# Optimization experiments

Hardware: AMD Instinct MI355X
Metric: run time of the kernel (lower is better)

Reference implementation:

```python
import jax, jax.numpy as jnp
import numpy as np

EPS = 1e-5
P = 2  # polynomial kernel degree


def setup_inputs() -> dict:
    key = jax.random.key(0)
    k1, k2, k3 = jax.random.split(key, 3)
    b, t, h, d = 2, 2048, 8, 64
    Q = jax.random.normal(k1, (b, t, h, d), jnp.float32)
    K = jax.random.normal(k2, (b, t, h, d), jnp.float32)
    V = jax.random.normal(k3, (b, t, h, d), jnp.float32)
    return {"Q": Q, "K": K, "V": V, "chunk_count": 16}


def reference(Q, K, V, chunk_count):
    b, t, h, d = Q.shape
    dv = V.shape[-1]
    c = chunk_count
    n = t // c  # tokens per chunk

    def to_chunked(X):
        # [b, t, h, d] -> [c, b, h, n, d]
        return X.reshape(b, c, n, h, X.shape[-1]).transpose(1, 0, 3, 2, 4)

    Qc, Kc, Vc = to_chunked(Q), to_chunked(K), to_chunked(V)

    # ---- per-chunk states: s = K^T K, S = sum_n (K_n outer K_n) outer V_n ----
    s_loc = jnp.einsum('cbhni,cbhnj->cbhij', Kc, Kc)                 # [c,b,h,d,d]
    S_loc = jnp.einsum('cbhni,cbhnj,cbhnv->cbhijv', Kc, Kc, Vc)      # [c,b,h,d,d,dv]
    # inclusive cumulative merge over chunks
    S = jnp.cumsum(S_loc, axis=0)
    s = jnp.cumsum(s_loc, axis=0)

    # ---- local within-chunk masked quadratic attention ----
    D = jnp.einsum('cbhqi,cbhki->cbhqk', Qc, Kc)                     # [c,b,h,n,n]
    C = D ** P
    mask = jnp.tril(jnp.ones((n, n), dtype=bool))
    B = jnp.where(mask, C, 0.0)
    Y = jnp.einsum('cbhqk,cbhkv->cbhqv', B, Vc)                      # [c,b,h,n,dv]
    Z = B.sum(-1) + EPS                                              # [c,b,h,n]

    # ---- cross-chunk contribution: chunk i>0 attends to state of chunks <i ----
    Qp = Qc[1:]
    Sp, sp = S[:-1], s[:-1]
    num = jnp.einsum('cbhni,cbhnj,cbhijv->cbhnv', Qp, Qp, Sp)
    den = jnp.einsum('cbhni,cbhnj,cbhij->cbhn', Qp, Qp, sp)
    Y = Y.at[1:].add(num)
    Z = Z.at[1:].add(den)

    out = (Y / Z[..., None]).transpose(1, 0, 3, 2, 4).reshape(b, t, h, dv)
    return out
```

## Files before the change

### kernel.cpp

```cpp
#include <hip/hip_runtime.h>
#include <hip/hip_fp16.h>

typedef __attribute__((ext_vector_type(8))) _Float16 f16x8;
typedef __attribute__((ext_vector_type(4))) _Float16 f16x4;
typedef __attribute__((ext_vector_type(8))) unsigned short u16x8;
typedef __attribute__((ext_vector_type(4))) float f32x4;

constexpr int NT = 256;
constexpr int TILE_SHORTS = 4096;

__device__ __forceinline__ int swzoff(int row, int c) {
    return row * 64 + ((c ^ (row & 7)) << 3);
}
__device__ __forceinline__ unsigned short f2h_u(float x) {
    return __half_as_ushort(__float2half(x));
}

__global__ __launch_bounds__(256, 4) void prepass(
    const float* __restrict__ Kg, const float* __restrict__ Vg,
    unsigned short* __restrict__ Kw, unsigned short* __restrict__ Vw)
{
    __shared__ __align__(16) float Vl[64 * 68];
    const int tile = blockIdx.x;
    const int bh   = blockIdx.y;
    const int b = bh >> 3, h = bh & 7;
    const int tid = threadIdx.x;
    const size_t gbase = (((size_t)b * 2048 + tile * 64) * 8 + h) * 64;

    #pragma unroll
    for (int j = 0; j < 4; ++j) {
        int id = j * 256 + tid, row = id >> 4, c4 = id & 15;
        *(float4*)&Vl[row * 68 + c4 * 4] =
            *(const float4*)&Vg[gbase + (size_t)row * 512 + c4 * 4];
    }

    unsigned short* Ko = Kw + (size_t)(bh * 32 + tile) * TILE_SHORTS;
    #pragma unroll
    for (int j = 0; j < 2; ++j) {
        int id = j * 256 + tid, row = id >> 3, c = id & 7;
        const float* src = &Kg[gbase + (size_t)row * 512 + c * 8];
        float4 x = *(const float4*)src, y = *(const float4*)(src + 4);
        u16x8 o;
        o[0] = f2h_u(x.x); o[1] = f2h_u(x.y); o[2] = f2h_u(x.z); o[3] = f2h_u(x.w);
        o[4] = f2h_u(y.x); o[5] = f2h_u(y.y); o[6] = f2h_u(y.z); o[7] = f2h_u(y.w);
        *(u16x8*)&Ko[swzoff(row, c)] = o;
    }
    __syncthreads();

    unsigned short* Vo = Vw + (size_t)(bh * 32 + tile) * TILE_SHORTS;
    #pragma unroll
    for (int j = 0; j < 2; ++j) {
        int id = j * 256 + tid, vrow = id >> 3, g = id & 7;
        u16x8 o;
        #pragma unroll
        for (int jj = 0; jj < 8; ++jj) {
            int kk = ((g & 1) * 2 + (jj >> 2)) * 16 + (g >> 1) * 4 + (jj & 3);
            o[jj] = f2h_u(Vl[kk * 68 + vrow]);
        }
        *(u16x8*)&Vo[swzoff(vrow, g)] = o;
    }
}

__global__ __launch_bounds__(NT, 3) void attn_pow2_f16(
    const float* __restrict__ Qg,
    const unsigned short* __restrict__ Kw, const unsigned short* __restrict__ Vw,
    float* __restrict__ Og)
{
    __shared__ __align__(16) unsigned short lds[4 * TILE_SHORTS];
    unsigned short* const Kb = lds;
    unsigned short* const Vb = lds + 2 * TILE_SHORTS;
    const int tid  = threadIdx.x;
    const int lane = tid & 63;
    const int wave = tid >> 6;
    const int a    = lane & 15;
    const int quad = lane >> 4;
    const int m0   = wave * 16;

    int r0 = (int)blockIdx.x;
    int wr = (r0 < 256) ? r0 : (767 - r0);
    const int qt = 31 - (wr >> 4);
    const int bh = wr & 15;
    const int b = bh >> 3, h = bh & 7;
    const int q0 = qt * 64;

    f16x8 bQ[2];
    {
        const size_t qrowbase = (((size_t)b * 2048 + q0 + m0 + a) * 8 + h) * 64;
        #pragma unroll
        for (int ks = 0; ks < 2; ++ks) {
            const float* src = &Qg[qrowbase + ks * 32 + quad * 8];
            float4 x = *(const float4*)src, y = *(const float4*)(src + 4);
            u16x8 o;
            o[0] = f2h_u(x.x); o[1] = f2h_u(x.y); o[2] = f2h_u(x.z); o[3] = f2h_u(x.w);
            o[4] = f2h_u(y.x); o[5] = f2h_u(y.y); o[6] = f2h_u(y.z); o[7] = f2h_u(y.w);
            bQ[ks] = __builtin_bit_cast(f16x8, o);
        }
    }

    const unsigned short* Ktiles = Kw + (size_t)bh * 32 * TILE_SHORTS;
    const unsigned short* Vtiles = Vw + (size_t)bh * 32 * TILE_SHORTS;

    u16x8 rK[2], rV[2];
    auto gload = [&](int kt) {
        const u16x8* kg = (const u16x8*)(Ktiles + (size_t)kt * TILE_SHORTS);
        const u16x8* vg = (const u16x8*)(Vtiles + (size_t)kt * TILE_SHORTS);
        rK[0] = kg[tid * 2]; rK[1] = kg[tid * 2 + 1];
        rV[0] = vg[tid * 2]; rV[1] = vg[tid * 2 + 1];
    };
    gload(0);

    f32x4 oacc[4];
    #pragma unroll
    for (int n = 0; n < 4; ++n) oacc[n] = (f32x4){0.f, 0.f, 0.f, 0.f};
    float den_l = 0.f;

    union U8 { u16x8 u; f16x4 q[2]; };

    for (int kt = 0; kt <= qt; ++kt) {
        const int buf = kt & 1;
        u16x8* kd = (u16x8*)(Kb + buf * TILE_SHORTS);
        u16x8* vd = (u16x8*)(Vb + buf * TILE_SHORTS);
        kd[tid * 2] = rK[0]; kd[tid * 2 + 1] = rK[1];
        vd[tid * 2] = rV[0]; vd[tid * 2 + 1] = rV[1];
        __syncthreads();
        if (kt < qt) gload(kt + 1);

        const unsigned short* Kc = Kb + buf * TILE_SHORTS;
        const unsigned short* Vc = Vb + buf * TILE_SHORTS;

        f32x4 sacc[4];
        #pragma unroll
        for (int s = 0; s < 4; ++s) sacc[s] = (f32x4){0.f, 0.f, 0.f, 0.f};
        #pragma unroll
        for (int s = 0; s < 4; ++s) {
            #pragma unroll
            for (int ks = 0; ks < 2; ++ks) {
                f16x8 aK = *(const f16x8*)&Kc[swzoff(s * 16 + a, ks * 4 + quad)];
                sacc[s] = __builtin_amdgcn_mfma_f32_16x16x32_f16(aK, bQ[ks], sacc[s], 0, 0, 0);
            }
        }

        const bool diag = (kt == qt);
        f16x4 aS[4];
        #pragma unroll
        for (int s = 0; s < 4; ++s) {
            float p[4];
            #pragma unroll
            for (int r = 0; r < 4; ++r) {
                float d0 = sacc[s][r];
                float v = d0 * d0;
                if (diag && (s * 16 + quad * 4 + r) > (m0 + a)) v = 0.f;
                p[r] = v;
            }
            den_l += (p[0] + p[1]) + (p[2] + p[3]);
            aS[s] = (f16x4){(_Float16)p[0], (_Float16)p[1], (_Float16)p[2], (_Float16)p[3]};
        }

        #pragma unroll
        for (int n = 0; n < 4; ++n) {
            const int vrow = n * 16 + a;
            U8 va, vb;
            va.u = *(const u16x8*)&Vc[swzoff(vrow, quad * 2)];
            vb.u = *(const u16x8*)&Vc[swzoff(vrow, quad * 2 + 1)];
            oacc[n] = __builtin_amdgcn_mfma_f32_16x16x16f16(aS[0], va.q[0], oacc[n], 0, 0, 0);
            oacc[n] = __builtin_amdgcn_mfma_f32_16x16x16f16(aS[1], va.q[1], oacc[n], 0, 0, 0);
            oacc[n] = __builtin_amdgcn_mfma_f32_16x16x16f16(aS[2], vb.q[0], oacc[n], 0, 0, 0);
            oacc[n] = __builtin_amdgcn_mfma_f32_16x16x16f16(aS[3], vb.q[1], oacc[n], 0, 0, 0);
        }
    }

    den_l += __shfl_xor(den_l, 16);
    den_l += __shfl_xor(den_l, 32);

    float invz[4];
    #pragma unroll
    for (int r = 0; r < 4; ++r) {
        float dq = __shfl(den_l, quad * 4 + r);
        invz[r] = 1.0f / (dq + 1e-5f);
    }

    #pragma unroll
    for (int n = 0; n < 4; ++n) {
        #pragma unroll
        for (int r = 0; r < 4; ++r) {
            int t = q0 + m0 + quad * 4 + r;
            int v = n * 16 + a;
            Og[(((size_t)b * 2048 + t) * 8 + h) * 64 + v] = oacc[n][r] * invz[r];
        }
    }
}

extern "C" void kernel_launch(void* const* d_in, const int* in_sizes, int n_in,
                              void* d_out, int out_size, void* d_ws, size_t ws_size,
                              hipStream_t stream) {
    const float* Q = (const float*)d_in[0];
    const float* K = (const float*)d_in[1];
    const float* V = (const float*)d_in[2];
    float* O = (float*)d_out;
    unsigned short* Kw = (unsigned short*)d_ws;
    unsigned short* Vw = Kw + (size_t)16 * 32 * TILE_SHORTS;

    prepass<<<dim3(32, 16), 256, 0, stream>>>(K, V, Kw, Vw);
    attn_pow2_f16<<<dim3(512), NT, 0, stream>>>(Q, Kw, Vw, O);
}
```

Baseline: 96.82 us.

## Load K/V fragments directly from global into registers, dropping LDS staging

The attention kernel no longer stages K and V tiles through shared memory with a barrier per tile. Each lane now reads its own MFMA operand fragments straight from the pre-swizzled global workspace into registers, using a two-slot register double buffer that prefetches the next tile while the current one is computed. This removes the LDS writes and reads and the __syncthreads per tile. In exchange every wave re-reads the full K/V tile from global or L2 (four times the previous traffic), register use rises sharply, and occupancy bounds drop from 3 to 2 blocks per SM.

```diff
diff --git a/kernel.cpp b/kernel.cpp
--- a/kernel.cpp
+++ b/kernel.cpp
@@ -61,14 +61,11 @@
     }
 }
 
-__global__ __launch_bounds__(NT, 3) void attn_pow2_f16(
+__global__ __launch_bounds__(NT, 2) void attn_pow2_f16(
     const float* __restrict__ Qg,
     const unsigned short* __restrict__ Kw, const unsigned short* __restrict__ Vw,
     float* __restrict__ Og)
 {
-    __shared__ __align__(16) unsigned short lds[4 * TILE_SHORTS];
-    unsigned short* const Kb = lds;
-    unsigned short* const Vb = lds + 2 * TILE_SHORTS;
     const int tid  = threadIdx.x;
     const int lane = tid & 63;
     const int wave = tid >> 6;
@@ -100,34 +97,34 @@
     const unsigned short* Ktiles = Kw + (size_t)bh * 32 * TILE_SHORTS;
     const unsigned short* Vtiles = Vw + (size_t)bh * 32 * TILE_SHORTS;
 
-    u16x8 rK[2], rV[2];
-    auto gload = [&](int kt) {
-        const u16x8* kg = (const u16x8*)(Ktiles + (size_t)kt * TILE_SHORTS);
-        const u16x8* vg = (const u16x8*)(Vtiles + (size_t)kt * TILE_SHORTS);
-        rK[0] = kg[tid * 2]; rK[1] = kg[tid * 2 + 1];
-        rV[0] = vg[tid * 2]; rV[1] = vg[tid * 2 + 1];
+    int koff[8], voff[8];
+    #pragma unroll
+    for (int s = 0; s < 4; ++s) {
+        koff[s * 2 + 0] = swzoff(s * 16 + a, quad);
+        koff[s * 2 + 1] = swzoff(s * 16 + a, 4 + quad);
+        voff[s * 2 + 0] = swzoff(s * 16 + a, quad * 2);
+        voff[s * 2 + 1] = swzoff(s * 16 + a, quad * 2 + 1);
+    }
+
+    u16x8 c0K[8], c0V[8], c1K[8], c1V[8];
+    auto gload = [&](int kt, u16x8 (&rk)[8], u16x8 (&rv)[8]) {
+        const unsigned short* kg = Ktiles + (size_t)kt * TILE_SHORTS;
+        const unsigned short* vg = Vtiles + (size_t)kt * TILE_SHORTS;
+        #pragma unroll
+        for (int i = 0; i < 8; ++i) {
+            rk[i] = *(const u16x8*)&kg[koff[i]];
+            rv[i] = *(const u16x8*)&vg[voff[i]];
+        }
     };
-    gload(0);
 
     f32x4 oacc[4];
     #pragma unroll
     for (int n = 0; n < 4; ++n) oacc[n] = (f32x4){0.f, 0.f, 0.f, 0.f};
     float den_l = 0.f;
 
-    union U8 { u16x8 u; f16x4 q[2]; };
-
-    for (int kt = 0; kt <= qt; ++kt) {
-        const int buf = kt & 1;
-        u16x8* kd = (u16x8*)(Kb + buf * TILE_SHORTS);
-        u16x8* vd = (u16x8*)(Vb + buf * TILE_SHORTS);
-        kd[tid * 2] = rK[0]; kd[tid * 2 + 1] = rK[1];
-        vd[tid * 2] = rV[0]; vd[tid * 2 + 1] = rV[1];
-        __syncthreads();
-        if (kt < qt) gload(kt + 1);
-
-        const unsigned short* Kc = Kb + buf * TILE_SHORTS;
-        const unsigned short* Vc = Vb + buf * TILE_SHORTS;
-
+    union U8 { u16x8 u; f16x4 q[2]; f16x8 f; };
+
+    auto compute = [&](const u16x8 (&rk)[8], const u16x8 (&rv)[8], bool diag) {
         f32x4 sacc[4];
         #pragma unroll
         for (int s = 0; s < 4; ++s) sacc[s] = (f32x4){0.f, 0.f, 0.f, 0.f};
@@ -135,12 +132,10 @@
         for (int s = 0; s < 4; ++s) {
             #pragma unroll
             for (int ks = 0; ks < 2; ++ks) {
-                f16x8 aK = *(const f16x8*)&Kc[swzoff(s * 16 + a, ks * 4 + quad)];
-                sacc[s] = __builtin_amdgcn_mfma_f32_16x16x32_f16(aK, bQ[ks], sacc[s], 0, 0, 0);
+                U8 ak; ak.u = rk[s * 2 + ks];
+                sacc[s] = __builtin_amdgcn_mfma_f32_16x16x32_f16(ak.f, bQ[ks], sacc[s], 0, 0, 0);
             }
         }
-
-        const bool diag = (kt == qt);
         f16x4 aS[4];
         #pragma unroll
         for (int s = 0; s < 4; ++s) {
@@ -155,17 +150,25 @@
             den_l += (p[0] + p[1]) + (p[2] + p[3]);
             aS[s] = (f16x4){(_Float16)p[0], (_Float16)p[1], (_Float16)p[2], (_Float16)p[3]};
         }
-
         #pragma unroll
         for (int n = 0; n < 4; ++n) {
-            const int vrow = n * 16 + a;
             U8 va, vb;
-            va.u = *(const u16x8*)&Vc[swzoff(vrow, quad * 2)];
-            vb.u = *(const u16x8*)&Vc[swzoff(vrow, quad * 2 + 1)];
+            va.u = rv[n * 2 + 0];
+            vb.u = rv[n * 2 + 1];
             oacc[n] = __builtin_amdgcn_mfma_f32_16x16x16f16(aS[0], va.q[0], oacc[n], 0, 0, 0);
             oacc[n] = __builtin_amdgcn_mfma_f32_16x16x16f16(aS[1], va.q[1], oacc[n], 0, 0, 0);
             oacc[n] = __builtin_amdgcn_mfma_f32_16x16x16f16(aS[2], vb.q[0], oacc[n], 0, 0, 0);
             oacc[n] = __builtin_amdgcn_mfma_f32_16x16x16f16(aS[3], vb.q[1], oacc[n], 0, 0, 0);
+        }
+    };
+
+    gload(0, c0K, c0V);
+    for (int kt = 0; kt <= qt; kt += 2) {
+        if (kt + 1 <= qt) gload(kt + 1, c1K, c1V);
+        compute(c0K, c0V, kt == qt);
+        if (kt + 1 <= qt) {
+            if (kt + 2 <= qt) gload(kt + 2, c0K, c0V);
+            compute(c1K, c1V, kt + 1 == qt);
         }
     }
 
```

Result: slower. 102.4 us (+5.8%).
